# Optimization experiments

Measured on AMD Instinct MI355X. Metric: run time of the kernel, lower is better.

## Reference

```python
import jax, jax.numpy as jnp
import numpy as np


def setup_inputs() -> dict:
    key = jax.random.key(0)
    k1, _ = jax.random.split(key)
    N, H, CH, T = 4, 8, 64, 2048
    qkv = jax.random.normal(k1, (N, H * 3 * CH, T), dtype=jnp.float32)
    rescale = jnp.ones((1,), dtype=jnp.float32)
    return {"qkv": qkv, "rescale": rescale, "n_heads": H}


def reference(qkv, rescale, n_heads):
    bs, width, length = qkv.shape
    ch = width // (3 * n_heads)
    # [N, H*3*C, T] -> [N*H, 3*C, T] -> three [N*H, C, T]
    qkv_h = qkv.reshape(bs * n_heads, 3 * ch, length)
    q, k, v = qkv_h[:, :ch], qkv_h[:, ch:2 * ch], qkv_h[:, 2 * ch:]
    scale = 1.0 / jnp.sqrt(jnp.sqrt(jnp.float32(ch)))
    # scores: [B*H, T, S]
    weight = jnp.einsum('bct,bcs->bts', q * scale, k * scale)
    weight = jax.nn.softmax(weight.astype(jnp.float32) * rescale[0], axis=-1).astype(qkv.dtype)
    a = jnp.einsum('bts,bcs->bct', weight, v)  # [B*H, C, T]
    return a.reshape(bs, n_heads * ch, length)
```

## Files before the change

kernel.cpp:

```cpp
#include <hip/hip_runtime.h>
#include <stdint.h>

typedef _Float16 half8 __attribute__((ext_vector_type(8)));
typedef _Float16 half4 __attribute__((ext_vector_type(4)));
typedef __fp16   fp16x2 __attribute__((ext_vector_type(2)));
typedef float    floatx4 __attribute__((ext_vector_type(4)));
typedef unsigned uintx2 __attribute__((ext_vector_type(2)));

#define T_LEN 2048
#define CH 64
#define BH 32
#define QTILE 128
#define LDP 72
#define FRAG_BH 131072

__global__ __launch_bounds__(256, 2)
void prep_kernel(const float* __restrict__ qkv, const float* __restrict__ rescale,
                 _Float16* __restrict__ ws)
{
    __shared__ _Float16 Qs[64][LDP];
    __shared__ _Float16 Ks[64][LDP];
    __shared__ _Float16 Vs[64][LDP];

    const int tid  = threadIdx.x;
    const int bh   = blockIdx.y;
    const int tile = blockIdx.x;
    const int x0   = tile * 64;

    const float qscale = 0.125f * 1.4426950408889634f * rescale[0];

    const float* qp = qkv + (size_t)(bh >> 3) * (1536 * T_LEN)
                          + (size_t)(bh & 7) * (192 * T_LEN);
    const float* kp = qp + 64 * T_LEN;
    const float* vp = qp + 128 * T_LEN;

    {
        const int a4 = (tid & 15) * 4;
        const int c4 = (tid >> 4) * 4;
        float4 rq[4], rk[4];
#pragma unroll
        for (int i = 0; i < 4; ++i) {
            rq[i] = *(const float4*)(qp + (size_t)(c4 + i) * T_LEN + x0 + a4);
            rk[i] = *(const float4*)(kp + (size_t)(c4 + i) * T_LEN + x0 + a4);
        }
#pragma unroll
        for (int j = 0; j < 4; ++j) {
            half4 hq, hk;
#pragma unroll
            for (int i = 0; i < 4; ++i) {
                hq[i] = (_Float16)((&rq[i].x)[j] * qscale);
                hk[i] = (_Float16)((&rk[i].x)[j]);
            }
            *(half4*)&Qs[a4 + j][c4] = hq;
            *(half4*)&Ks[a4 + j][c4] = hk;
        }
        const int s4 = (tid & 15) * 4;
        const int cv = tid >> 4;
#pragma unroll
        for (int i = 0; i < 4; ++i) {
            const int c = cv + 16 * i;
            float4 r = *(const float4*)(vp + (size_t)c * T_LEN + x0 + s4);
            half4 h; h[0]=(_Float16)r.x; h[1]=(_Float16)r.y; h[2]=(_Float16)r.z; h[3]=(_Float16)r.w;
            *(half4*)&Vs[c][s4] = h;
        }
    }
    __syncthreads();

    const int lane = tid & 63, wave = tid >> 6;
    const int l15 = lane & 15, quad = lane >> 4;
    _Float16* qf = ws;
    _Float16* kf = ws + (size_t)BH * FRAG_BH;
    _Float16* vf = ws + (size_t)2 * BH * FRAG_BH;

#pragma unroll
    for (int ks = 0; ks < 2; ++ks) {
        half8 hq = *(const half8*)&Qs[wave * 16 + l15][ks * 32 + quad * 8];
        half8 hk = *(const half8*)&Ks[wave * 16 + l15][ks * 32 + quad * 8];
        const size_t gqk = (((size_t)bh * 128 + tile * 4 + wave) * 2 + ks) * 512 + lane * 8;
        *(half8*)(qf + gqk) = hq;
        *(half8*)(kf + gqk) = hk;
    }
#pragma unroll
    for (int ct = 0; ct < 4; ++ct) {
        half4 hv = *(const half4*)&Vs[ct * 16 + l15][wave * 16 + quad * 4];
        *(half4*)(vf + (size_t)bh * FRAG_BH
                     + ((size_t)(tile * 4 + wave) * 4 + ct) * 256 + lane * 4) = hv;
    }
}

__device__ __forceinline__ void gload16(const _Float16* g, _Float16* l) {
    __builtin_amdgcn_global_load_lds(
        (const __attribute__((address_space(1))) void*)g,
        (__attribute__((address_space(3))) void*)l, 16, 0, 0);
}

__global__ __launch_bounds__(256, 2)
void attn_kernel(const _Float16* __restrict__ ws, float* __restrict__ out)
{
    __shared__ _Float16 Kb[2][4096];
    __shared__ _Float16 Vb[2][4096];

    const int tid  = threadIdx.x;
    const int wave = tid >> 6;
    const int lane = tid & 63;
    const int l15  = lane & 15;
    const int quad = lane >> 4;

    const int bid  = blockIdx.x;
    const int xcd  = bid & 7;
    const int slot = bid >> 3;
    const int bh   = (slot >> 4) * 8 + xcd;
    const int tile = slot & 15;
    const int t0   = tile * QTILE;

    const _Float16* qf = ws;
    const _Float16* kf = ws + (size_t)BH * FRAG_BH;
    const _Float16* vf = ws + (size_t)2 * BH * FRAG_BH;
    float* op = out + (size_t)bh * (CH * T_LEN);

    const _Float16* ktile = kf + (size_t)bh * FRAG_BH;
    const _Float16* vtile = vf + (size_t)bh * FRAG_BH;

    auto stage = [&](int st, int buf) {
        const _Float16* kg = ktile + (size_t)st * 4096 + wave * 1024 + lane * 8;
        const _Float16* vg = vtile + (size_t)st * 4096 + wave * 1024 + lane * 8;
        _Float16* kl = &Kb[buf][wave * 1024];
        _Float16* vl = &Vb[buf][wave * 1024];
        gload16(kg,       kl);
        gload16(kg + 512, kl + 512);
        gload16(vg,       vl);
        gload16(vg + 512, vl + 512);
    };

    half8 bq[2][2];
#pragma unroll
    for (int tb = 0; tb < 2; ++tb)
#pragma unroll
        for (int ks = 0; ks < 2; ++ks)
            bq[tb][ks] = *(const half8*)(qf +
                (((size_t)bh * 128 + tile * 8 + wave * 2 + tb) * 2 + ks) * 512 + lane * 8);

    const floatx4 fzero = {0.f, 0.f, 0.f, 0.f};
    floatx4 oacc[4][2];
#pragma unroll
    for (int ct = 0; ct < 4; ++ct)
#pragma unroll
        for (int tb = 0; tb < 2; ++tb) oacc[ct][tb] = fzero;
    float lsum[2] = {0.f, 0.f};

    half8 ak[4][2];
    half4 bv[4][4];

    auto read_ak = [&](int buf) {
#pragma unroll
        for (int mt = 0; mt < 4; ++mt)
#pragma unroll
            for (int ks = 0; ks < 2; ++ks)
                ak[mt][ks] = *(const half8*)&Kb[buf][(mt * 2 + ks) * 512 + lane * 8];
    };
    auto read_bv = [&](int buf) {
#pragma unroll
        for (int mt = 0; mt < 4; ++mt)
#pragma unroll
            for (int ct = 0; ct < 4; ++ct)
                bv[mt][ct] = *(const half4*)&Vb[buf][mt * 1024 + ct * 256 + lane * 4];
    };

    auto body = [&]() {
#pragma unroll
        for (int mt = 0; mt < 4; ++mt) {
            floatx4 s0 = fzero, s1 = fzero;
#pragma unroll
            for (int ks = 0; ks < 2; ++ks) {
                s0 = __builtin_amdgcn_mfma_f32_16x16x32_f16(ak[mt][ks], bq[0][ks], s0, 0, 0, 0);
                s1 = __builtin_amdgcn_mfma_f32_16x16x32_f16(ak[mt][ks], bq[1][ks], s1, 0, 0, 0);
            }
            float a0 = __builtin_amdgcn_exp2f(s0[0]);
            float a1 = __builtin_amdgcn_exp2f(s0[1]);
            float a2 = __builtin_amdgcn_exp2f(s0[2]);
            float a3 = __builtin_amdgcn_exp2f(s0[3]);
            float b0 = __builtin_amdgcn_exp2f(s1[0]);
            float b1 = __builtin_amdgcn_exp2f(s1[1]);
            float b2 = __builtin_amdgcn_exp2f(s1[2]);
            float b3 = __builtin_amdgcn_exp2f(s1[3]);
            lsum[0] += (a0 + a1) + (a2 + a3);
            lsum[1] += (b0 + b1) + (b2 + b3);
            uintx2 u0, u1;
            u0[0] = __builtin_bit_cast(unsigned, __builtin_amdgcn_cvt_pkrtz(a0, a1));
            u0[1] = __builtin_bit_cast(unsigned, __builtin_amdgcn_cvt_pkrtz(a2, a3));
            u1[0] = __builtin_bit_cast(unsigned, __builtin_amdgcn_cvt_pkrtz(b0, b1));
            u1[1] = __builtin_bit_cast(unsigned, __builtin_amdgcn_cvt_pkrtz(b2, b3));
            half4 p0 = __builtin_bit_cast(half4, u0);
            half4 p1 = __builtin_bit_cast(half4, u1);
#pragma unroll
            for (int ct = 0; ct < 4; ++ct) {
                oacc[ct][0] = __builtin_amdgcn_mfma_f32_16x16x16f16(
                    bv[mt][ct], p0, oacc[ct][0], 0, 0, 0);
                oacc[ct][1] = __builtin_amdgcn_mfma_f32_16x16x16f16(
                    bv[mt][ct], p1, oacc[ct][1], 0, 0, 0);
            }
        }
    };

    stage(0, 0);
    __syncthreads();
    read_ak(0);
    read_bv(0);
    stage(1, 1);

    for (int st = 0; st < 32; ++st) {
        const int cur = st & 1;
        if (st >= 1 && st < 31) stage(st + 1, cur ^ 1);
        body();
        if (st < 31) {
            __syncthreads();
            read_ak(cur ^ 1);
            read_bv(cur ^ 1);
        }
    }

    float linv[2];
#pragma unroll
    for (int tb = 0; tb < 2; ++tb) {
        float v = lsum[tb];
        v += __shfl_xor(v, 16, 64);
        v += __shfl_xor(v, 32, 64);
        linv[tb] = 1.0f / v;
    }
#pragma unroll
    for (int tb = 0; tb < 2; ++tb) {
        const int t = t0 + wave * 32 + tb * 16 + l15;
#pragma unroll
        for (int ct = 0; ct < 4; ++ct)
#pragma unroll
            for (int r = 0; r < 4; ++r)
                op[(size_t)(ct * 16 + quad * 4 + r) * T_LEN + t] = oacc[ct][tb][r] * linv[tb];
    }
}

extern "C" void kernel_launch(void* const* d_in, const int* in_sizes, int n_in,
                              void* d_out, int out_size, void* d_ws, size_t ws_size,
                              hipStream_t stream) {
    const float* qkv     = (const float*)d_in[0];
    const float* rescale = (const float*)d_in[1];
    float* out = (float*)d_out;
    _Float16* ws = (_Float16*)d_ws;

    prep_kernel<<<dim3(32, BH), dim3(256), 0, stream>>>(qkv, rescale, ws);
    attn_kernel<<<dim3(T_LEN / QTILE * BH), dim3(256), 0, stream>>>(ws, out);
}
```

Measured before the change: 133.1 us.

## Split attention block into 8 waves each owning 16 query rows

```diff
diff --git a/kernel.cpp b/kernel.cpp
--- a/kernel.cpp
+++ b/kernel.cpp
@@ -94,7 +94,7 @@
         (__attribute__((address_space(3))) void*)l, 16, 0, 0);
 }
 
-__global__ __launch_bounds__(256, 2)
+__global__ __launch_bounds__(512, 4)
 void attn_kernel(const _Float16* __restrict__ ws, float* __restrict__ out)
 {
     __shared__ _Float16 Kb[2][4096];
@@ -122,31 +122,23 @@
     const _Float16* vtile = vf + (size_t)bh * FRAG_BH;
 
     auto stage = [&](int st, int buf) {
-        const _Float16* kg = ktile + (size_t)st * 4096 + wave * 1024 + lane * 8;
-        const _Float16* vg = vtile + (size_t)st * 4096 + wave * 1024 + lane * 8;
-        _Float16* kl = &Kb[buf][wave * 1024];
-        _Float16* vl = &Vb[buf][wave * 1024];
-        gload16(kg,       kl);
-        gload16(kg + 512, kl + 512);
-        gload16(vg,       vl);
-        gload16(vg + 512, vl + 512);
-    };
-
-    half8 bq[2][2];
-#pragma unroll
-    for (int tb = 0; tb < 2; ++tb)
-#pragma unroll
-        for (int ks = 0; ks < 2; ++ks)
-            bq[tb][ks] = *(const half8*)(qf +
-                (((size_t)bh * 128 + tile * 8 + wave * 2 + tb) * 2 + ks) * 512 + lane * 8);
+        const _Float16* kg = ktile + (size_t)st * 4096 + wave * 512 + lane * 8;
+        const _Float16* vg = vtile + (size_t)st * 4096 + wave * 512 + lane * 8;
+        gload16(kg, &Kb[buf][wave * 512]);
+        gload16(vg, &Vb[buf][wave * 512]);
+    };
+
+    half8 bq[2];
+#pragma unroll
+    for (int ks = 0; ks < 2; ++ks)
+        bq[ks] = *(const half8*)(qf +
+            (((size_t)bh * 128 + tile * 8 + wave) * 2 + ks) * 512 + lane * 8);
 
     const floatx4 fzero = {0.f, 0.f, 0.f, 0.f};
-    floatx4 oacc[4][2];
-#pragma unroll
-    for (int ct = 0; ct < 4; ++ct)
-#pragma unroll
-        for (int tb = 0; tb < 2; ++tb) oacc[ct][tb] = fzero;
-    float lsum[2] = {0.f, 0.f};
+    floatx4 oacc[4];
+#pragma unroll
+    for (int ct = 0; ct < 4; ++ct) oacc[ct] = fzero;
+    float lsum = 0.f;
 
     half8 ak[4][2];
     half4 bv[4][4];
@@ -169,36 +161,23 @@
     auto body = [&]() {
 #pragma unroll
         for (int mt = 0; mt < 4; ++mt) {
-            floatx4 s0 = fzero, s1 = fzero;
-#pragma unroll
-            for (int ks = 0; ks < 2; ++ks) {
-                s0 = __builtin_amdgcn_mfma_f32_16x16x32_f16(ak[mt][ks], bq[0][ks], s0, 0, 0, 0);
-                s1 = __builtin_amdgcn_mfma_f32_16x16x32_f16(ak[mt][ks], bq[1][ks], s1, 0, 0, 0);
-            }
+            floatx4 s0 = fzero;
+#pragma unroll
+            for (int ks = 0; ks < 2; ++ks)
+                s0 = __builtin_amdgcn_mfma_f32_16x16x32_f16(ak[mt][ks], bq[ks], s0, 0, 0, 0);
             float a0 = __builtin_amdgcn_exp2f(s0[0]);
             float a1 = __builtin_amdgcn_exp2f(s0[1]);
             float a2 = __builtin_amdgcn_exp2f(s0[2]);
             float a3 = __builtin_amdgcn_exp2f(s0[3]);
-            float b0 = __builtin_amdgcn_exp2f(s1[0]);
-            float b1 = __builtin_amdgcn_exp2f(s1[1]);
-            float b2 = __builtin_amdgcn_exp2f(s1[2]);
-            float b3 = __builtin_amdgcn_exp2f(s1[3]);
-            lsum[0] += (a0 + a1) + (a2 + a3);
-            lsum[1] += (b0 + b1) + (b2 + b3);
-            uintx2 u0, u1;
+            lsum += (a0 + a1) + (a2 + a3);
+            uintx2 u0;
             u0[0] = __builtin_bit_cast(unsigned, __builtin_amdgcn_cvt_pkrtz(a0, a1));
             u0[1] = __builtin_bit_cast(unsigned, __builtin_amdgcn_cvt_pkrtz(a2, a3));
-            u1[0] = __builtin_bit_cast(unsigned, __builtin_amdgcn_cvt_pkrtz(b0, b1));
-            u1[1] = __builtin_bit_cast(unsigned, __builtin_amdgcn_cvt_pkrtz(b2, b3));
             half4 p0 = __builtin_bit_cast(half4, u0);
-            half4 p1 = __builtin_bit_cast(half4, u1);
-#pragma unroll
-            for (int ct = 0; ct < 4; ++ct) {
-                oacc[ct][0] = __builtin_amdgcn_mfma_f32_16x16x16f16(
-                    bv[mt][ct], p0, oacc[ct][0], 0, 0, 0);
-                oacc[ct][1] = __builtin_amdgcn_mfma_f32_16x16x16f16(
-                    bv[mt][ct], p1, oacc[ct][1], 0, 0, 0);
-            }
+#pragma unroll
+            for (int ct = 0; ct < 4; ++ct)
+                oacc[ct] = __builtin_amdgcn_mfma_f32_16x16x16f16(
+                    bv[mt][ct], p0, oacc[ct], 0, 0, 0);
         }
     };
 
@@ -219,23 +198,16 @@
         }
     }
 
-    float linv[2];
-#pragma unroll
-    for (int tb = 0; tb < 2; ++tb) {
-        float v = lsum[tb];
-        v += __shfl_xor(v, 16, 64);
-        v += __shfl_xor(v, 32, 64);
-        linv[tb] = 1.0f / v;
-    }
-#pragma unroll
-    for (int tb = 0; tb < 2; ++tb) {
-        const int t = t0 + wave * 32 + tb * 16 + l15;
-#pragma unroll
-        for (int ct = 0; ct < 4; ++ct)
-#pragma unroll
-            for (int r = 0; r < 4; ++r)
-                op[(size_t)(ct * 16 + quad * 4 + r) * T_LEN + t] = oacc[ct][tb][r] * linv[tb];
-    }
+    float v = lsum;
+    v += __shfl_xor(v, 16, 64);
+    v += __shfl_xor(v, 32, 64);
+    const float linv = 1.0f / v;
+    const int t = t0 + wave * 16 + l15;
+#pragma unroll
+    for (int ct = 0; ct < 4; ++ct)
+#pragma unroll
+        for (int r = 0; r < 4; ++r)
+            op[(size_t)(ct * 16 + quad * 4 + r) * T_LEN + t] = oacc[ct][r] * linv;
 }
 
 extern "C" void kernel_launch(void* const* d_in, const int* in_sizes, int n_in,
@@ -247,5 +219,5 @@
     _Float16* ws = (_Float16*)d_ws;
 
     prep_kernel<<<dim3(32, BH), dim3(256), 0, stream>>>(qkv, rescale, ws);
-    attn_kernel<<<dim3(T_LEN / QTILE * BH), dim3(256), 0, stream>>>(ws, out);
-}
+    attn_kernel<<<dim3(T_LEN / QTILE * BH), dim3(512), 0, stream>>>(ws, out);
+}
```

Measured after the change: 136.6 us. 1.03x slower.
